# Performance work log

Measured on AMD Instinct MI355X. Metric: run time of the kernel, lower is better.

## Reference

```python
import jax, jax.numpy as jnp
import numpy as np

NUM_ACT = 64
SIZE = 51  # odd -> even=False branch
RANGE = 4.0
GRID = 2.0 * RANGE / (SIZE - 1)  # 0.16


def setup_inputs() -> dict:
    key = jax.random.key(0)
    k1, k2 = jax.random.split(key)
    x = jax.random.normal(k1, (32, NUM_ACT, 128, 128), dtype=jnp.float32)
    # coefficients initialized like 'relu' init would be, but random works for a
    # numerical baseline; keep values bounded like real spline coeffs
    coefficients_vect = jax.random.normal(k2, (NUM_ACT * SIZE,), dtype=jnp.float32)
    scaling_coeffs_vect = jnp.ones((1, NUM_ACT, 1, 1), dtype=jnp.float32)
    return {"x": x, "coefficients_vect": coefficients_vect,
            "scaling_coeffs_vect": scaling_coeffs_vect}


def reference(x, coefficients_vect, scaling_coeffs_vect):
    grid = jnp.float32(GRID)
    # zero-knot index of each activation in the flat coefficient vector
    zero_knot = (jnp.arange(NUM_ACT, dtype=jnp.int32) * SIZE + SIZE // 2)  # [C]
    xs = x * scaling_coeffs_vect  # [N,C,H,W]
    max_range = GRID * (SIZE // 2 - 1)  # odd size: no grid/2 shift
    x_clamped = jnp.clip(xs, -GRID * (SIZE // 2), max_range)
    floored = jnp.floor(x_clamped / grid)
    # NOTE: fracs uses the UNclamped xs, matching the torch code
    fracs = xs / grid - floored
    idx = (zero_knot[None, :, None, None] + floored).astype(jnp.int32)
    # gather two neighboring coefficients and linearly interpolate
    out = coefficients_vect[idx + 1] * fracs + coefficients_vect[idx] * (1.0 - fracs)
    return out / scaling_coeffs_vect
```

## Files before the change

kernel.cpp:

```cpp
#include <hip/hip_runtime.h>

#define NUM_ACT 64
#define SPLINE_SIZE 51

typedef float f32x4 __attribute__((ext_vector_type(4)));

__global__ __launch_bounds__(256) void linear_spline_kernel(
    const f32x4* __restrict__ x4,
    const float* __restrict__ coef,
    const float* __restrict__ scale,
    f32x4* __restrict__ out4)
{
    __shared__ float lcoef[SPLINE_SIZE];

    int c = (blockIdx.x >> 3) & (NUM_ACT - 1);

    if (threadIdx.x < SPLINE_SIZE)
        lcoef[threadIdx.x] = coef[c * SPLINE_SIZE + threadIdx.x];

    float s  = scale[c];
    float rs = 1.0f / s;

    __syncthreads();

    const float inv_grid = 6.25f;

    int base = blockIdx.x * 512 + threadIdx.x;

#pragma unroll
    for (int j = 0; j < 2; ++j) {
        int i = base + j * 256;
        f32x4 xv = __builtin_nontemporal_load(&x4[i]);
        f32x4 ov;
#pragma unroll
        for (int k = 0; k < 4; ++k) {
            float xs = xv[k] * s;
            float t  = xs * inv_grid;
            int fl = (int)floorf(t);
            fl = min(max(fl, -(SPLINE_SIZE / 2)), SPLINE_SIZE / 2 - 1);
            float fr = t - (float)fl;
            int li = fl + SPLINE_SIZE / 2;
            float c0 = lcoef[li];
            float c1 = lcoef[li + 1];
            ov[k] = (c1 * fr + c0 * (1.0f - fr)) * rs;
        }
        __builtin_nontemporal_store(ov, &out4[i]);
    }
}

extern "C" void kernel_launch(void* const* d_in, const int* in_sizes, int n_in,
                              void* d_out, int out_size, void* d_ws, size_t ws_size,
                              hipStream_t stream) {
    const float* x     = (const float*)d_in[0];
    const float* coef  = (const float*)d_in[1];
    const float* scale = (const float*)d_in[2];
    float* out = (float*)d_out;

    int n  = in_sizes[0];
    int n4 = n >> 2;
    int grid = n4 / 512;

    linear_spline_kernel<<<grid, 256, 0, stream>>>(
        (const f32x4*)x, coef, scale, (f32x4*)out);
}
```

Measured before the change: 221.6 us.

## Process one full plane per block with software-prefetched loads and folded scaling

Each block now handles a whole 128x128 channel plane (4096 float4s) instead of 512 float4s. It issues four float4 loads ahead of the compute of the previous group, so more memory requests are in flight per thread. The coefficient table is pre-multiplied by 1/scale and the scale and grid factors are merged into one multiply, which removes per-element arithmetic. This cuts the grid to 2048 blocks, which may lower occupancy and latency hiding, and the extra live registers raise register pressure.

```diff
diff --git a/kernel.cpp b/kernel.cpp
--- a/kernel.cpp
+++ b/kernel.cpp
@@ -13,38 +13,54 @@
 {
     __shared__ float lcoef[SPLINE_SIZE];
 
-    int c = (blockIdx.x >> 3) & (NUM_ACT - 1);
+    const int plane = blockIdx.x;
+    const int c = plane & (NUM_ACT - 1);
+
+    const float s  = scale[c];
+    const float rs = 1.0f / s;
 
     if (threadIdx.x < SPLINE_SIZE)
-        lcoef[threadIdx.x] = coef[c * SPLINE_SIZE + threadIdx.x];
+        lcoef[threadIdx.x] = coef[c * SPLINE_SIZE + threadIdx.x] * rs;
 
-    float s  = scale[c];
-    float rs = 1.0f / s;
+    const float sg = s * 6.25f;
 
     __syncthreads();
 
-    const float inv_grid = 6.25f;
+    const int base = plane * 4096 + threadIdx.x;
 
-    int base = blockIdx.x * 512 + threadIdx.x;
+    f32x4 cur[4], nxt[4];
+#pragma unroll
+    for (int k = 0; k < 4; ++k)
+        cur[k] = __builtin_nontemporal_load(&x4[base + k * 256]);
 
 #pragma unroll
-    for (int j = 0; j < 2; ++j) {
-        int i = base + j * 256;
-        f32x4 xv = __builtin_nontemporal_load(&x4[i]);
-        f32x4 ov;
+    for (int g = 0; g < 4; ++g) {
+        if (g < 3) {
+#pragma unroll
+            for (int k = 0; k < 4; ++k)
+                nxt[k] = __builtin_nontemporal_load(&x4[base + (g + 1) * 1024 + k * 256]);
+        }
 #pragma unroll
         for (int k = 0; k < 4; ++k) {
-            float xs = xv[k] * s;
-            float t  = xs * inv_grid;
-            int fl = (int)floorf(t);
-            fl = min(max(fl, -(SPLINE_SIZE / 2)), SPLINE_SIZE / 2 - 1);
-            float fr = t - (float)fl;
-            int li = fl + SPLINE_SIZE / 2;
-            float c0 = lcoef[li];
-            float c1 = lcoef[li + 1];
-            ov[k] = (c1 * fr + c0 * (1.0f - fr)) * rs;
+            f32x4 xv = cur[k];
+            f32x4 ov;
+#pragma unroll
+            for (int e = 0; e < 4; ++e) {
+                float t = xv[e] * sg;
+                int fl = (int)floorf(t);
+                fl = min(max(fl, -(SPLINE_SIZE / 2)), SPLINE_SIZE / 2 - 1);
+                float fr = t - (float)fl;
+                int li = fl + SPLINE_SIZE / 2;
+                float c0 = lcoef[li];
+                float c1 = lcoef[li + 1];
+                ov[e] = c0 + (c1 - c0) * fr;
+            }
+            __builtin_nontemporal_store(ov, &out4[base + g * 1024 + k * 256]);
         }
-        __builtin_nontemporal_store(ov, &out4[i]);
+        if (g < 3) {
+#pragma unroll
+            for (int k = 0; k < 4; ++k) cur[k] = nxt[k];
+        }
     }
 }
 
@@ -56,10 +72,10 @@
     const float* scale = (const float*)d_in[2];
     float* out = (float*)d_out;
 
-    int n  = in_sizes[0];
-    int n4 = n >> 2;
-    int grid = n4 / 512;
+    int n      = in_sizes[0];
+    int n4     = n >> 2;
+    int planes = n4 / 4096;
 
-    linear_spline_kernel<<<grid, 256, 0, stream>>>(
+    linear_spline_kernel<<<planes, 256, 0, stream>>>(
         (const f32x4*)x, coef, scale, (f32x4*)out);
 }
```

New measurement: 225.3 us. No clear change (+1.7%).
